# Performance work log

Hardware: AMD Instinct MI355X
Metric: run time of the kernel (lower is better)

## Reference

```python
import jax, jax.numpy as jnp
import numpy as np

B, S, D = 4, 2048, 1024  # batch, seq_len, d_model (h=16 but unused due to source bug)


def setup_inputs() -> dict:
    key = jax.random.key(0)
    ks = jax.random.split(key, 12)
    scale = 1.0 / np.sqrt(D)
    return {
        "q": jax.random.normal(ks[0], (B, S, D), jnp.float32),
        "k": jax.random.normal(ks[1], (B, S, D), jnp.float32),
        "v": jax.random.normal(ks[2], (B, S, D), jnp.float32),
        "mask": jnp.ones((1, 1, S, S), dtype=bool),
        "Wq": jax.random.normal(ks[3], (D, D), jnp.float32) * scale,
        "bq": jnp.zeros((D,), jnp.float32),
        "Wk": jax.random.normal(ks[4], (D, D), jnp.float32) * scale,
        "bk": jnp.zeros((D,), jnp.float32),
        "Wv": jax.random.normal(ks[5], (D, D), jnp.float32) * scale,
        "bv": jnp.zeros((D,), jnp.float32),
        "Wo": jax.random.normal(ks[6], (D, D), jnp.float32) * scale,
        "bo": jnp.zeros((D,), jnp.float32),
    }


def reference(q, k, v, mask, Wq, bq, Wk, bk, Wv, bv, Wo, bo):
    # Faithful to source bugs: head split discarded (attention over full d_model),
    # mask discarded (masked_fill out-of-place), dropout=0 (identity).
    query = q @ Wq + bq  # [B,S,D]
    key = k @ Wk + bk
    value = v @ Wv + bv
    d_k = query.shape[-1]  # = d_model due to the bug
    scores = jnp.einsum('bqd,bkd->bqk', query, key) / jnp.sqrt(jnp.float32(d_k))
    attn = jax.nn.softmax(scores, axis=-1)  # [B,S,S]
    x = jnp.einsum('bqk,bkd->bqd', attn, value)  # [B,S,D]
    # source: x.transpose(1,2).contiguous().view(B,-1,D) -> layout permutation
    b, s, d = x.shape
    x = jnp.swapaxes(x, 1, 2).reshape(b, s, d)
    return x @ Wo + bo
```

## Files before the change

### kernel.cpp

```cpp
#include <hip/hip_runtime.h>
#include <hip/hip_bf16.h>
#include <stdint.h>

typedef __attribute__((ext_vector_type(8))) short short8;
typedef __attribute__((ext_vector_type(4))) float f32x4;
typedef const __attribute__((address_space(1))) uint32_t* gas1_t;
typedef __attribute__((address_space(3))) uint32_t* las3_t;

__device__ __forceinline__ short f2bf(float f) {
  uint32_t u = __builtin_bit_cast(uint32_t, f);
  u += 0x7fffu + ((u >> 16) & 1u);
  return (short)(u >> 16);
}
__device__ __forceinline__ float bf2f(short s) {
  return __builtin_bit_cast(float, ((uint32_t)(uint16_t)s) << 16);
}

__global__ __launch_bounds__(256) void cvt_qkv_k(const float* __restrict__ q,
    const float* __restrict__ k, const float* __restrict__ v,
    short* __restrict__ dst) {
  const long long n = 8388608LL;
  const float* src = (blockIdx.z == 0) ? q : (blockIdx.z == 1) ? k : v;
  long long i = ((long long)blockIdx.x * 256 + threadIdx.x) * 8;
  float4 a = *(const float4*)(src + i);
  float4 b = *(const float4*)(src + i + 4);
  short8 o;
  o[0]=f2bf(a.x); o[1]=f2bf(a.y); o[2]=f2bf(a.z); o[3]=f2bf(a.w);
  o[4]=f2bf(b.x); o[5]=f2bf(b.y); o[6]=f2bf(b.z); o[7]=f2bf(b.w);
  *(short8*)(dst + (long long)blockIdx.z * n + i) = o;
}

__global__ __launch_bounds__(256) void bias_gather_k(const float* b0, const float* b1,
    const float* b2, const float* b3, float* __restrict__ dst) {
  int i = blockIdx.x * 256 + threadIdx.x;
  if (i >= 4096) return;
  int z = i >> 10, j = i & 1023;
  const float* s = (z==0)?b0:(z==1)?b1:(z==2)?b2:b3;
  dst[i] = s[j];
}

__global__ __launch_bounds__(256) void wt_cvt_k(const float* w0, const float* w1,
    const float* w2, const float* w3, short* __restrict__ dst) {
  __shared__ float t[32][33];
  const float* W = (blockIdx.z==0)?w0:(blockIdx.z==1)?w1:(blockIdx.z==2)?w2:w3;
  short* D = dst + (long long)blockIdx.z * 1048576LL;
  int n0 = blockIdx.x * 32, k0 = blockIdx.y * 32;
  int tx = threadIdx.x, ty = threadIdx.y;
  #pragma unroll
  for (int i = 0; i < 4; ++i)
    t[ty + 8*i][tx] = W[(long long)(k0 + ty + 8*i) * 1024 + n0 + tx];
  __syncthreads();
  #pragma unroll
  for (int i = 0; i < 4; ++i)
    D[(long long)(n0 + ty + 8*i) * 1024 + k0 + tx] = f2bf(t[tx][ty + 8*i]);
}

__global__ __launch_bounds__(256) void softmax_bf_k(short* __restrict__ SP) {
  short* sp = SP + (long long)blockIdx.x * 2048;
  const int t = threadIdx.x;
  short8 sv = *(const short8*)(sp + t*8);
  float v[8];
  #pragma unroll
  for (int j = 0; j < 8; ++j) v[j] = bf2f(sv[j]);
  float m = v[0];
  #pragma unroll
  for (int j = 1; j < 8; ++j) m = fmaxf(m, v[j]);
  #pragma unroll
  for (int off = 32; off > 0; off >>= 1) m = fmaxf(m, __shfl_down(m, off, 64));
  __shared__ float rmax[4], rsum[4];
  int wv = t >> 6, ln = t & 63;
  if (ln == 0) rmax[wv] = m;
  __syncthreads();
  m = fmaxf(fmaxf(rmax[0], rmax[1]), fmaxf(rmax[2], rmax[3]));
  float e[8], sum = 0.f;
  #pragma unroll
  for (int j = 0; j < 8; ++j) { e[j] = exp2f((v[j] - m) * 1.44269504f); sum += e[j]; }
  #pragma unroll
  for (int off = 32; off > 0; off >>= 1) sum += __shfl_down(sum, off, 64);
  if (ln == 0) rsum[wv] = sum;
  __syncthreads();
  float inv = 1.0f / (rsum[0] + rsum[1] + rsum[2] + rsum[3]);
  short8 o;
  #pragma unroll
  for (int j = 0; j < 8; ++j) o[j] = f2bf(e[j] * inv);
  *(short8*)(sp + t*8) = o;
}

#define MFMA16(d, a_, b_) d = __builtin_amdgcn_mfma_f32_16x16x32_bf16(a_, b_, d, 0, 0, 0)
#define XCD_DECODE(gxs_, gys_) \
  const int nwg = (int)gridDim.x; \
  const int wg = ((int)blockIdx.x & 7) * (nwg >> 3) + ((int)blockIdx.x >> 3); \
  const int bxi = wg & ((1 << (gxs_)) - 1); \
  const int byi = (wg >> (gxs_)) & ((1 << (gys_)) - 1); \
  const int z = wg >> ((gxs_) + (gys_));

template<int OUT_BF16>
__global__ __launch_bounds__(512, 2) void gemm2_k(const short* __restrict__ A,
    const short* __restrict__ Bt, void* __restrict__ Cv,
    const float* __restrict__ bias,
    int K, int lda, int ldb, int ldc,
    long long sA, long long sB, long long sC, long long sBias,
    float scale, int gxs, int gys)
{
  __shared__ __align__(16) short lds[3][16384];
  XCD_DECODE(gxs, gys);
  A  += (long long)z * sA;
  Bt += (long long)z * sB;
  const int bm = byi * 256;
  const int bn = bxi * 256;
  const int tid  = threadIdx.x;
  const int w    = tid >> 6, lane = tid & 63;
  const int wr   = w >> 2,   wc   = w & 3;
  const int lr   = lane & 15, lk  = lane >> 4;

  const int rsw  = (lk ^ ((lr >> 1) & 3)) * 8;
  const int srow = w * 16 + (lane >> 2);
  const int sg   = ((lane & 3) ^ ((lane >> 3) & 3)) * 8;
  const short* gA[2]; const short* gB[2];
  #pragma unroll
  for (int i = 0; i < 2; ++i) {
    gA[i] = A  + (long long)(bm + i*128 + srow) * lda + sg;
    gB[i] = Bt + (long long)(bn + i*128 + srow) * ldb + sg;
  }

  #define STGA2(buf, i, kt) \
    __builtin_amdgcn_global_load_lds((gas1_t)(gA[i] + (long long)(kt)*32), \
        (las3_t)&lds[buf][(i)*4096 + w*512], 16, 0, 0)
  #define STGB2(buf, i, kt) \
    __builtin_amdgcn_global_load_lds((gas1_t)(gB[i] + (long long)(kt)*32), \
        (las3_t)&lds[buf][8192 + (i)*4096 + w*512], 16, 0, 0)
  #define RDA2(buf, mi) (*(const short8*)&lds[buf][(wr*128 + (mi)*16 + lr)*32 + rsw])
  #define RDB2(buf, ni) (*(const short8*)&lds[buf][8192 + (wc*64 + (ni)*16 + lr)*32 + rsw])

  f32x4 acc[8][4] = {};
  const int nt = K >> 5;

  STGA2(0, 0, 0); STGA2(0, 1, 0); STGB2(0, 0, 0); STGB2(0, 1, 0);
  STGA2(1, 0, 1); STGA2(1, 1, 1); STGB2(1, 0, 1); STGB2(1, 1, 1);
  asm volatile("s_waitcnt vmcnt(4)" ::: "memory");
  __builtin_amdgcn_s_barrier();
  __builtin_amdgcn_sched_barrier(0);

  int b = 0, nb = 2;
  for (int g = 0; g < nt; ++g) {
    short8 aR[8], bR[4];
    #pragma unroll
    for (int mi = 0; mi < 8; ++mi) aR[mi] = RDA2(b, mi);
    #pragma unroll
    for (int ni = 0; ni < 4; ++ni) bR[ni] = RDB2(b, ni);
    if (g + 2 < nt) { STGA2(nb, 0, g+2); STGA2(nb, 1, g+2);
                      STGB2(nb, 0, g+2); STGB2(nb, 1, g+2); }
    #pragma unroll
    for (int mi = 0; mi < 8; ++mi)
      #pragma unroll
      for (int ni = 0; ni < 4; ++ni)
        MFMA16(acc[mi][ni], aR[mi], bR[ni]);
    if (g + 2 < nt)      asm volatile("s_waitcnt vmcnt(4)" ::: "memory");
    else if (g + 1 < nt) asm volatile("s_waitcnt vmcnt(0)" ::: "memory");
    __builtin_amdgcn_s_barrier();
    __builtin_amdgcn_sched_barrier(0);
    b  = (b  == 2) ? 0 : b  + 1;
    nb = (nb == 2) ? 0 : nb + 1;
  }

  const float* bz = bias ? (bias + (long long)z * sBias) : nullptr;
  #pragma unroll
  for (int mi = 0; mi < 8; ++mi) {
    const int row = bm + wr*128 + mi*16 + lk*4;
    #pragma unroll
    for (int ni = 0; ni < 4; ++ni) {
      const int col = bn + wc*64 + ni*16 + lr;
      const float bval = bz ? bz[col] : 0.f;
      #pragma unroll
      for (int r = 0; r < 4; ++r) {
        float val = acc[mi][ni][r] * scale + bval;
        if (OUT_BF16)
          ((short*)Cv)[(long long)z*sC + (long long)(row + r) * ldc + col] = f2bf(val);
        else
          ((float*)Cv)[(long long)z*sC + (long long)(row + r) * ldc + col] = val;
      }
    }
  }
  #undef STGA2
  #undef STGB2
  #undef RDA2
  #undef RDB2
}

template<int OUT_BF16, int BIAS_ROW>
__global__ __launch_bounds__(512, 2) void gemm4_k(const short* __restrict__ A,
    const short* __restrict__ Bt, void* __restrict__ Cv,
    const float* __restrict__ bias,
    int K, int lda, int ldb, int ldc,
    long long sA, long long sB, long long sC, long long sBias,
    float scale, int gxs, int gys)
{
  __shared__ __align__(16) short lds[3][24576];
  XCD_DECODE(gxs, gys);
  A  += (long long)z * sA;
  Bt += (long long)z * sB;
  const int bm = byi * 256;
  const int bn = bxi * 128;
  const int tid  = threadIdx.x;
  const int w    = tid >> 6, lane = tid & 63;
  const int wr   = w >> 1,   wc   = w & 1;
  const int lr   = lane & 15, lk  = lane >> 4;

  const int rsw0 = ((lk    ) ^ (lr & 7)) * 8;
  const int rsw1 = ((lk + 4) ^ (lr & 7)) * 8;
  const int srow = w * 8 + (lane >> 3);
  const int swc  = ((lane & 7) ^ ((lane >> 3) & 7)) * 8;
  const short* gA[4]; const short* gB[2];
  #pragma unroll
  for (int i = 0; i < 4; ++i)
    gA[i] = A + (long long)(bm + i*64 + srow) * lda + swc;
  #pragma unroll
  for (int i = 0; i < 2; ++i)
    gB[i] = Bt + (long long)(bn + i*64 + srow) * ldb + swc;

  #define STGA(buf, i, kt) \
    __builtin_amdgcn_global_load_lds((gas1_t)(gA[i] + (long long)(kt)*64), \
        (las3_t)&lds[buf][(i)*4096 + w*512], 16, 0, 0)
  #define STGB(buf, i, kt) \
    __builtin_amdgcn_global_load_lds((gas1_t)(gB[i] + (long long)(kt)*64), \
        (las3_t)&lds[buf][16384 + (i)*4096 + w*512], 16, 0, 0)
  #define RDA4(buf, mi, ks) (*(const short8*)&lds[buf][(wr*64 + (mi)*16 + lr)*64 + ((ks) ? rsw1 : rsw0)])
  #define RDB4(buf, ni, ks) (*(const short8*)&lds[buf][16384 + (wc*64 + (ni)*16 + lr)*64 + ((ks) ? rsw1 : rsw0)])

  f32x4 acc[4][4] = {};
  const int nt = K >> 6;

  STGA(0, 0, 0); STGA(0, 2, 0); STGB(0, 0, 0);
  STGB(0, 1, 0); STGA(0, 1, 0); STGA(0, 3, 0);
  STGA(1, 0, 1); STGA(1, 2, 1); STGB(1, 0, 1);
  STGB(1, 1, 1); STGA(1, 1, 1); STGA(1, 3, 1);
  asm volatile("s_waitcnt vmcnt(6)" ::: "memory");
  __builtin_amdgcn_s_barrier();
  __builtin_amdgcn_sched_barrier(0);

  int b = 0, nb = 2;
  for (int g = 0; g < nt; ++g) {
    short8 aR[4][2], bR[4][2];
    #pragma unroll
    for (int mi = 0; mi < 4; ++mi) { aR[mi][0] = RDA4(b, mi, 0); aR[mi][1] = RDA4(b, mi, 1); }
    #pragma unroll
    for (int ni = 0; ni < 4; ++ni) { bR[ni][0] = RDB4(b, ni, 0); bR[ni][1] = RDB4(b, ni, 1); }
    if (g + 2 < nt) { STGA(nb, 0, g+2); STGA(nb, 2, g+2); STGB(nb, 0, g+2);
                      STGB(nb, 1, g+2); STGA(nb, 1, g+2); STGA(nb, 3, g+2); }
    #pragma unroll
    for (int mi = 0; mi < 4; ++mi)
      #pragma unroll
      for (int ni = 0; ni < 4; ++ni) {
        MFMA16(acc[mi][ni], aR[mi][0], bR[ni][0]);
        MFMA16(acc[mi][ni], aR[mi][1], bR[ni][1]);
      }
    if (g + 2 < nt)      asm volatile("s_waitcnt vmcnt(6)" ::: "memory");
    else if (g + 1 < nt) asm volatile("s_waitcnt vmcnt(0)" ::: "memory");
    __builtin_amdgcn_s_barrier();
    __builtin_amdgcn_sched_barrier(0);
    b  = (b  == 2) ? 0 : b  + 1;
    nb = (nb == 2) ? 0 : nb + 1;
  }

  const float* bz = bias;
  #pragma unroll
  for (int mi = 0; mi < 4; ++mi) {
    const int row = bm + wr*64 + mi*16 + lk*4;
    #pragma unroll
    for (int ni = 0; ni < 4; ++ni) {
      const int col = bn + wc*64 + ni*16 + lr;
      const float bcol = (bz && !BIAS_ROW) ? bz[(long long)z*sBias + col] : 0.f;
      #pragma unroll
      for (int r = 0; r < 4; ++r) {
        float bval = BIAS_ROW ? bz[row + r] : bcol;
        float val = acc[mi][ni][r] * scale + bval;
        if (OUT_BF16)
          ((short*)Cv)[(long long)z*sC + (long long)(row + r) * ldc + col] = f2bf(val);
        else
          ((float*)Cv)[(long long)z*sC + (long long)(row + r) * ldc + col] = val;
      }
    }
  }
  #undef STGA
  #undef STGB
  #undef RDA4
  #undef RDB4
}

extern "C" void kernel_launch(void* const* d_in, const int* in_sizes, int n_in,
                              void* d_out, int out_size, void* d_ws, size_t ws_size,
                              hipStream_t stream) {
  const float* q  = (const float*)d_in[0];
  const float* k  = (const float*)d_in[1];
  const float* v  = (const float*)d_in[2];
  const float* Wq = (const float*)d_in[4];
  const float* bq = (const float*)d_in[5];
  const float* Wk = (const float*)d_in[6];
  const float* bk = (const float*)d_in[7];
  const float* Wv = (const float*)d_in[8];
  const float* bv = (const float*)d_in[9];
  const float* Wo = (const float*)d_in[10];
  const float* bo = (const float*)d_in[11];

  char* w = (char*)d_ws;
  short* Wt     = (short*)(w);
  float* biasb  = (float*)(w + 8388608);
  short* QKV    = (short*)(w + 8404992);
  short* qkvbf  = (short*)(w + 58736640);
  short* P      = (short*)(w + 58736640);
  short* Vt     = (short*)(w + 109068288);
  short* xt     = (short*)(w + 125845504);

  short* Qp = QKV;
  short* Kp = QKV + 8388608LL;
  short* vbf = qkvbf + 16777216LL;

  cvt_qkv_k<<<dim3(4096,1,3), 256, 0, stream>>>(q, k, v, qkvbf);
  bias_gather_k<<<dim3(16), 256, 0, stream>>>(bq, bk, bv, bo, biasb);
  wt_cvt_k<<<dim3(32,32,4), dim3(32,8), 0, stream>>>(Wq, Wk, Wv, Wo, Wt);

  gemm2_k<1><<<256, 512, 0, stream>>>(qkvbf, Wt, QKV, biasb,
      1024, 1024, 1024, 1024, 8388608LL, 1048576LL, 8388608LL, 1024LL, 1.0f, 2, 5);

  gemm4_k<1,1><<<256, 512, 0, stream>>>(Wt + 2097152LL, vbf, Vt, biasb + 2048,
      1024, 1024, 1024, 8192, 0LL, 0LL, 0LL, 0LL, 1.0f, 6, 2);

  gemm2_k<1><<<256, 512, 0, stream>>>(Qp, Kp, P, nullptr,
      1024, 1024, 1024, 2048, 2097152LL, 2097152LL, 4194304LL, 0LL, 0.03125f, 3, 3);

  softmax_bf_k<<<dim3(8192), 256, 0, stream>>>(P);

  gemm4_k<1,0><<<256, 512, 0, stream>>>(Vt, P, xt, nullptr,
      2048, 8192, 2048, 2048, 2048LL, 4194304LL, 2097152LL, 0LL, 1.0f, 4, 2);

  gemm4_k<0,0><<<256, 512, 0, stream>>>(xt, Wt + 3145728LL, (float*)d_out,
      biasb + 3072, 1024, 1024, 1024, 1024, 2097152LL, 0LL, 2097152LL, 0LL, 1.0f, 3, 3);
}
```

Measured before the change: 207.9 us.

## Fuse fp32-to-bf16 input conversion into QKV projection GEMM loads

Removes the separate cvt_qkv_k pass over q, k and v. New GEMM variants load the fp32 activations straight into LDS and convert them to bf16 in registers before the MFMA. This avoids writing and re-reading about 50 MB of bf16 intermediates. In exchange each GEMM moves twice the bytes per A/B tile through LDS and does conversion work in the inner loop, which may cost occupancy or MFMA throughput.

```diff
diff --git a/kernel.cpp b/kernel.cpp
--- a/kernel.cpp
+++ b/kernel.cpp
@@ -15,19 +15,11 @@
 __device__ __forceinline__ float bf2f(short s) {
   return __builtin_bit_cast(float, ((uint32_t)(uint16_t)s) << 16);
 }
-
-__global__ __launch_bounds__(256) void cvt_qkv_k(const float* __restrict__ q,
-    const float* __restrict__ k, const float* __restrict__ v,
-    short* __restrict__ dst) {
-  const long long n = 8388608LL;
-  const float* src = (blockIdx.z == 0) ? q : (blockIdx.z == 1) ? k : v;
-  long long i = ((long long)blockIdx.x * 256 + threadIdx.x) * 8;
-  float4 a = *(const float4*)(src + i);
-  float4 b = *(const float4*)(src + i + 4);
-  short8 o;
-  o[0]=f2bf(a.x); o[1]=f2bf(a.y); o[2]=f2bf(a.z); o[3]=f2bf(a.w);
-  o[4]=f2bf(b.x); o[5]=f2bf(b.y); o[6]=f2bf(b.z); o[7]=f2bf(b.w);
-  *(short8*)(dst + (long long)blockIdx.z * n + i) = o;
+__device__ __forceinline__ short8 cvt8(float4 a, float4 b) {
+  short8 s;
+  s[0]=f2bf(a.x); s[1]=f2bf(a.y); s[2]=f2bf(a.z); s[3]=f2bf(a.w);
+  s[4]=f2bf(b.x); s[5]=f2bf(b.y); s[6]=f2bf(b.z); s[7]=f2bf(b.w);
+  return s;
 }
 
 __global__ __launch_bounds__(256) void bias_gather_k(const float* b0, const float* b1,
@@ -187,6 +179,179 @@
   #undef RDB2
 }
 
+__global__ __launch_bounds__(512, 2) void gemm2f_k(
+    const float* __restrict__ A0p, const float* __restrict__ A1p,
+    const short* __restrict__ Bt, short* __restrict__ C,
+    const float* __restrict__ bias,
+    int K, int lda, int ldb, int ldc,
+    long long sB, long long sC, long long sBias,
+    float scale, int gxs, int gys)
+{
+  __shared__ __align__(16) short lds[3][24576];
+  XCD_DECODE(gxs, gys);
+  const float* Af = z ? A1p : A0p;
+  const int bm = byi * 256;
+  const int bn = bxi * 256;
+  const int tid  = threadIdx.x;
+  const int w    = tid >> 6, lane = tid & 63;
+  const int wr   = w >> 2,   wc   = w & 3;
+  const int lr   = lane & 15, lk  = lane >> 4;
+
+  const int sarow = w * 8 + (lane >> 3);
+  const int sag   = ((lane & 7) ^ ((lane >> 3) & 7)) * 4;
+  const int sbrow = w * 16 + (lane >> 2);
+  const int sbg   = ((lane & 3) ^ ((lane >> 3) & 3)) * 8;
+  const int rswb  = (lk ^ ((lr >> 1) & 3)) * 8;
+  const float* gAf[4]; const short* gB[2];
+  #pragma unroll
+  for (int i = 0; i < 4; ++i)
+    gAf[i] = Af + (long long)(bm + i*64 + sarow) * lda + sag;
+  #pragma unroll
+  for (int i = 0; i < 2; ++i)
+    gB[i] = Bt + (long long)z * sB + (long long)(bn + i*128 + sbrow) * ldb + sbg;
+
+  #define STGAF(buf, i, kt) \
+    __builtin_amdgcn_global_load_lds((gas1_t)(gAf[i] + (long long)(kt)*32), \
+        (las3_t)&lds[buf][(i)*4096 + w*512], 16, 0, 0)
+  #define STGBF(buf, i, kt) \
+    __builtin_amdgcn_global_load_lds((gas1_t)(gB[i] + (long long)(kt)*32), \
+        (las3_t)&lds[buf][16384 + (i)*4096 + w*512], 16, 0, 0)
+  #define RDAF(buf, mi, j) (*(const float4*)&lds[buf][(wr*128 + (mi)*16 + lr)*64 + ((2*lk + (j)) ^ (lr & 7))*8])
+  #define RDBF(buf, ni) (*(const short8*)&lds[buf][16384 + (wc*64 + (ni)*16 + lr)*32 + rswb])
+
+  f32x4 acc[8][4] = {};
+  const int nt = K >> 5;
+
+  STGAF(0,0,0); STGAF(0,1,0); STGAF(0,2,0); STGAF(0,3,0); STGBF(0,0,0); STGBF(0,1,0);
+  STGAF(1,0,1); STGAF(1,1,1); STGAF(1,2,1); STGAF(1,3,1); STGBF(1,0,1); STGBF(1,1,1);
+  asm volatile("s_waitcnt vmcnt(6)" ::: "memory");
+  __builtin_amdgcn_s_barrier();
+  __builtin_amdgcn_sched_barrier(0);
+
+  int b = 0, nb = 2;
+  for (int g = 0; g < nt; ++g) {
+    short8 aR[8], bR[4];
+    #pragma unroll
+    for (int mi = 0; mi < 8; ++mi) aR[mi] = cvt8(RDAF(b, mi, 0), RDAF(b, mi, 1));
+    #pragma unroll
+    for (int ni = 0; ni < 4; ++ni) bR[ni] = RDBF(b, ni);
+    if (g + 2 < nt) { STGAF(nb,0,g+2); STGAF(nb,1,g+2); STGAF(nb,2,g+2);
+                      STGAF(nb,3,g+2); STGBF(nb,0,g+2); STGBF(nb,1,g+2); }
+    #pragma unroll
+    for (int mi = 0; mi < 8; ++mi)
+      #pragma unroll
+      for (int ni = 0; ni < 4; ++ni)
+        MFMA16(acc[mi][ni], aR[mi], bR[ni]);
+    if (g + 2 < nt)      asm volatile("s_waitcnt vmcnt(6)" ::: "memory");
+    else if (g + 1 < nt) asm volatile("s_waitcnt vmcnt(0)" ::: "memory");
+    __builtin_amdgcn_s_barrier();
+    __builtin_amdgcn_sched_barrier(0);
+    b  = (b  == 2) ? 0 : b  + 1;
+    nb = (nb == 2) ? 0 : nb + 1;
+  }
+
+  const float* bz = bias + (long long)z * sBias;
+  #pragma unroll
+  for (int mi = 0; mi < 8; ++mi) {
+    const int row = bm + wr*128 + mi*16 + lk*4;
+    #pragma unroll
+    for (int ni = 0; ni < 4; ++ni) {
+      const int col = bn + wc*64 + ni*16 + lr;
+      const float bval = bz[col];
+      #pragma unroll
+      for (int r = 0; r < 4; ++r)
+        C[(long long)z*sC + (long long)(row + r) * ldc + col] = f2bf(acc[mi][ni][r] * scale + bval);
+    }
+  }
+  #undef STGAF
+  #undef STGBF
+  #undef RDAF
+  #undef RDBF
+}
+
+__global__ __launch_bounds__(512, 2) void gemm4f_k(
+    const short* __restrict__ A, const float* __restrict__ Btf,
+    short* __restrict__ C, const float* __restrict__ bias,
+    int K, int lda, int ldb, int ldc, float scale, int gxs, int gys)
+{
+  __shared__ __align__(16) short lds[3][16384];
+  XCD_DECODE(gxs, gys);
+  (void)z;
+  const int bm = byi * 256;
+  const int bn = bxi * 128;
+  const int tid  = threadIdx.x;
+  const int w    = tid >> 6, lane = tid & 63;
+  const int wr   = w >> 1,   wc   = w & 1;
+  const int lr   = lane & 15, lk  = lane >> 4;
+
+  const int sarow = w * 16 + (lane >> 2);
+  const int sag   = ((lane & 3) ^ ((lane >> 3) & 3)) * 8;
+  const int rswa  = (lk ^ ((lr >> 1) & 3)) * 8;
+  const int sbrow = w * 8 + (lane >> 3);
+  const int sbg   = ((lane & 7) ^ ((lane >> 3) & 7)) * 4;
+  const short* gA[2]; const float* gBf[2];
+  #pragma unroll
+  for (int i = 0; i < 2; ++i) {
+    gA[i]  = A   + (long long)(bm + i*128 + sarow) * lda + sag;
+    gBf[i] = Btf + (long long)(bn + i*64  + sbrow) * ldb + sbg;
+  }
+
+  #define STGA4(buf, i, kt) \
+    __builtin_amdgcn_global_load_lds((gas1_t)(gA[i] + (long long)(kt)*32), \
+        (las3_t)&lds[buf][(i)*4096 + w*512], 16, 0, 0)
+  #define STGB4(buf, i, kt) \
+    __builtin_amdgcn_global_load_lds((gas1_t)(gBf[i] + (long long)(kt)*32), \
+        (las3_t)&lds[buf][8192 + (i)*4096 + w*512], 16, 0, 0)
+  #define RDA4F(buf, mi) (*(const short8*)&lds[buf][(wr*64 + (mi)*16 + lr)*32 + rswa])
+  #define RDB4F(buf, ni, j) (*(const float4*)&lds[buf][8192 + (wc*64 + (ni)*16 + lr)*64 + ((2*lk + (j)) ^ (lr & 7))*8])
+
+  f32x4 acc[4][4] = {};
+  const int nt = K >> 5;
+
+  STGA4(0,0,0); STGA4(0,1,0); STGB4(0,0,0); STGB4(0,1,0);
+  STGA4(1,0,1); STGA4(1,1,1); STGB4(1,0,1); STGB4(1,1,1);
+  asm volatile("s_waitcnt vmcnt(4)" ::: "memory");
+  __builtin_amdgcn_s_barrier();
+  __builtin_amdgcn_sched_barrier(0);
+
+  int b = 0, nb = 2;
+  for (int g = 0; g < nt; ++g) {
+    short8 aR[4], bR[4];
+    #pragma unroll
+    for (int mi = 0; mi < 4; ++mi) aR[mi] = RDA4F(b, mi);
+    #pragma unroll
+    for (int ni = 0; ni < 4; ++ni) bR[ni] = cvt8(RDB4F(b, ni, 0), RDB4F(b, ni, 1));
+    if (g + 2 < nt) { STGA4(nb,0,g+2); STGA4(nb,1,g+2); STGB4(nb,0,g+2); STGB4(nb,1,g+2); }
+    #pragma unroll
+    for (int mi = 0; mi < 4; ++mi)
+      #pragma unroll
+      for (int ni = 0; ni < 4; ++ni)
+        MFMA16(acc[mi][ni], aR[mi], bR[ni]);
+    if (g + 2 < nt)      asm volatile("s_waitcnt vmcnt(4)" ::: "memory");
+    else if (g + 1 < nt) asm volatile("s_waitcnt vmcnt(0)" ::: "memory");
+    __builtin_amdgcn_s_barrier();
+    __builtin_amdgcn_sched_barrier(0);
+    b  = (b  == 2) ? 0 : b  + 1;
+    nb = (nb == 2) ? 0 : nb + 1;
+  }
+
+  #pragma unroll
+  for (int mi = 0; mi < 4; ++mi) {
+    const int row = bm + wr*64 + mi*16 + lk*4;
+    #pragma unroll
+    for (int ni = 0; ni < 4; ++ni) {
+      const int col = bn + wc*64 + ni*16 + lr;
+      #pragma unroll
+      for (int r = 0; r < 4; ++r)
+        C[(long long)(row + r) * ldc + col] = f2bf(acc[mi][ni][r] * scale + bias[row + r]);
+    }
+  }
+  #undef STGA4
+  #undef STGB4
+  #undef RDA4F
+  #undef RDB4F
+}
+
 template<int OUT_BF16, int BIAS_ROW>
 __global__ __launch_bounds__(512, 2) void gemm4_k(const short* __restrict__ A,
     const short* __restrict__ Bt, void* __restrict__ Cv,
@@ -306,24 +471,21 @@
   short* Wt     = (short*)(w);
   float* biasb  = (float*)(w + 8388608);
   short* QKV    = (short*)(w + 8404992);
-  short* qkvbf  = (short*)(w + 58736640);
   short* P      = (short*)(w + 58736640);
   short* Vt     = (short*)(w + 109068288);
   short* xt     = (short*)(w + 125845504);
 
   short* Qp = QKV;
   short* Kp = QKV + 8388608LL;
-  short* vbf = qkvbf + 16777216LL;
-
-  cvt_qkv_k<<<dim3(4096,1,3), 256, 0, stream>>>(q, k, v, qkvbf);
+
   bias_gather_k<<<dim3(16), 256, 0, stream>>>(bq, bk, bv, bo, biasb);
   wt_cvt_k<<<dim3(32,32,4), dim3(32,8), 0, stream>>>(Wq, Wk, Wv, Wo, Wt);
 
-  gemm2_k<1><<<256, 512, 0, stream>>>(qkvbf, Wt, QKV, biasb,
-      1024, 1024, 1024, 1024, 8388608LL, 1048576LL, 8388608LL, 1024LL, 1.0f, 2, 5);
-
-  gemm4_k<1,1><<<256, 512, 0, stream>>>(Wt + 2097152LL, vbf, Vt, biasb + 2048,
-      1024, 1024, 1024, 8192, 0LL, 0LL, 0LL, 0LL, 1.0f, 6, 2);
+  gemm2f_k<<<256, 512, 0, stream>>>(q, k, Wt, QKV, biasb,
+      1024, 1024, 1024, 1024, 1048576LL, 8388608LL, 1024LL, 1.0f, 2, 5);
+
+  gemm4f_k<<<256, 512, 0, stream>>>(Wt + 2097152LL, v, Vt, biasb + 2048,
+      1024, 1024, 1024, 8192, 1.0f, 6, 2);
 
   gemm2_k<1><<<256, 512, 0, stream>>>(Qp, Kp, P, nullptr,
       1024, 1024, 1024, 2048, 2097152LL, 2097152LL, 4194304LL, 0LL, 0.03125f, 3, 3);
```

Measured after the change: 218.9 us. +5.3%, slower.

## Rework gemm4 main loop to K=32 tiles with 4-stage ring and register double-buffering

Applied to the files above, without the earlier changes.

Replaces the 256x128 GEMM's 3-buffer K=64 LDS pipeline with a 4-buffer ring of K=32 tiles, a new XOR swizzle, and even/odd register double-buffering. The LDS reads for the next tile are issued before the MFMAs of the current one, so read latency overlaps with math. LDS use drops from 144KB to 96KB per block. The cost is twice as many barriers per unit of K, and the smaller per-iteration global loads may expose more load latency.

```diff
diff --git a/kernel.cpp b/kernel.cpp
--- a/kernel.cpp
+++ b/kernel.cpp
@@ -188,14 +188,14 @@
 }
 
 template<int OUT_BF16, int BIAS_ROW>
-__global__ __launch_bounds__(512, 2) void gemm4_k(const short* __restrict__ A,
+__global__ __launch_bounds__(512, 2) void gemm4r_k(const short* __restrict__ A,
     const short* __restrict__ Bt, void* __restrict__ Cv,
     const float* __restrict__ bias,
     int K, int lda, int ldb, int ldc,
     long long sA, long long sB, long long sC, long long sBias,
     float scale, int gxs, int gys)
 {
-  __shared__ __align__(16) short lds[3][24576];
+  __shared__ __align__(16) short lds[4][12288];
   XCD_DECODE(gxs, gys);
   A  += (long long)z * sA;
   Bt += (long long)z * sB;
@@ -206,60 +206,72 @@
   const int wr   = w >> 1,   wc   = w & 1;
   const int lr   = lane & 15, lk  = lane >> 4;
 
-  const int rsw0 = ((lk    ) ^ (lr & 7)) * 8;
-  const int rsw1 = ((lk + 4) ^ (lr & 7)) * 8;
-  const int srow = w * 8 + (lane >> 3);
-  const int swc  = ((lane & 7) ^ ((lane >> 3) & 7)) * 8;
-  const short* gA[4]; const short* gB[2];
-  #pragma unroll
-  for (int i = 0; i < 4; ++i)
-    gA[i] = A + (long long)(bm + i*64 + srow) * lda + swc;
-  #pragma unroll
-  for (int i = 0; i < 2; ++i)
-    gB[i] = Bt + (long long)(bn + i*64 + srow) * ldb + swc;
-
-  #define STGA(buf, i, kt) \
-    __builtin_amdgcn_global_load_lds((gas1_t)(gA[i] + (long long)(kt)*64), \
-        (las3_t)&lds[buf][(i)*4096 + w*512], 16, 0, 0)
-  #define STGB(buf, i, kt) \
-    __builtin_amdgcn_global_load_lds((gas1_t)(gB[i] + (long long)(kt)*64), \
-        (las3_t)&lds[buf][16384 + (i)*4096 + w*512], 16, 0, 0)
-  #define RDA4(buf, mi, ks) (*(const short8*)&lds[buf][(wr*64 + (mi)*16 + lr)*64 + ((ks) ? rsw1 : rsw0)])
-  #define RDB4(buf, ni, ks) (*(const short8*)&lds[buf][16384 + (wc*64 + (ni)*16 + lr)*64 + ((ks) ? rsw1 : rsw0)])
+  const int rsw  = (lk ^ ((lr >> 1) & 3)) * 8;
+  const int srow = w * 16 + (lane >> 2);
+  const int sg   = ((lane & 3) ^ ((lane >> 3) & 3)) * 8;
+  const short* gA[2]; const short* gB;
+  #pragma unroll
+  for (int h = 0; h < 2; ++h)
+    gA[h] = A + (long long)(bm + h*128 + srow) * lda + sg;
+  gB = Bt + (long long)(bn + srow) * ldb + sg;
+
+  #define STGAr(buf, h, kt) \
+    __builtin_amdgcn_global_load_lds((gas1_t)(gA[h] + (long long)(kt)*32), \
+        (las3_t)&lds[buf][(h)*4096 + w*512], 16, 0, 0)
+  #define STGBr(buf, kt) \
+    __builtin_amdgcn_global_load_lds((gas1_t)(gB + (long long)(kt)*32), \
+        (las3_t)&lds[buf][8192 + w*512], 16, 0, 0)
+  #define RDAr(buf, mi) (*(const short8*)&lds[buf][(wr*64 + (mi)*16 + lr)*32 + rsw])
+  #define RDBr(buf, ni) (*(const short8*)&lds[buf][8192 + (wc*64 + (ni)*16 + lr)*32 + rsw])
 
   f32x4 acc[4][4] = {};
-  const int nt = K >> 6;
-
-  STGA(0, 0, 0); STGA(0, 2, 0); STGB(0, 0, 0);
-  STGB(0, 1, 0); STGA(0, 1, 0); STGA(0, 3, 0);
-  STGA(1, 0, 1); STGA(1, 2, 1); STGB(1, 0, 1);
-  STGB(1, 1, 1); STGA(1, 1, 1); STGA(1, 3, 1);
-  asm volatile("s_waitcnt vmcnt(6)" ::: "memory");
+  const int nt = K >> 5;
+
+  STGAr(0, 0, 0); STGAr(0, 1, 0); STGBr(0, 0);
+  STGAr(1, 0, 1); STGAr(1, 1, 1); STGBr(1, 1);
+  asm volatile("s_waitcnt vmcnt(3)" ::: "memory");
   __builtin_amdgcn_s_barrier();
   __builtin_amdgcn_sched_barrier(0);
 
-  int b = 0, nb = 2;
-  for (int g = 0; g < nt; ++g) {
-    short8 aR[4][2], bR[4][2];
-    #pragma unroll
-    for (int mi = 0; mi < 4; ++mi) { aR[mi][0] = RDA4(b, mi, 0); aR[mi][1] = RDA4(b, mi, 1); }
-    #pragma unroll
-    for (int ni = 0; ni < 4; ++ni) { bR[ni][0] = RDB4(b, ni, 0); bR[ni][1] = RDB4(b, ni, 1); }
-    if (g + 2 < nt) { STGA(nb, 0, g+2); STGA(nb, 2, g+2); STGB(nb, 0, g+2);
-                      STGB(nb, 1, g+2); STGA(nb, 1, g+2); STGA(nb, 3, g+2); }
-    #pragma unroll
-    for (int mi = 0; mi < 4; ++mi)
-      #pragma unroll
-      for (int ni = 0; ni < 4; ++ni) {
-        MFMA16(acc[mi][ni], aR[mi][0], bR[ni][0]);
-        MFMA16(acc[mi][ni], aR[mi][1], bR[ni][1]);
+  short8 aE[4], bE[4], aO[4], bO[4];
+  #pragma unroll
+  for (int i = 0; i < 4; ++i) { aE[i] = RDAr(0, i); bE[i] = RDBr(0, i); }
+
+  for (int g = 0; g < nt; g += 2) {
+    {
+      const int bs = (g + 2) & 3;
+      if (g + 2 < nt) { STGAr(bs, 0, g+2); STGAr(bs, 1, g+2); STGBr(bs, g+2); }
+      if (g + 2 < nt)      asm volatile("s_waitcnt vmcnt(3)" ::: "memory");
+      else                 asm volatile("s_waitcnt vmcnt(0)" ::: "memory");
+      __builtin_amdgcn_s_barrier();
+      __builtin_amdgcn_sched_barrier(0);
+      const int br = (g + 1) & 3;
+      #pragma unroll
+      for (int i = 0; i < 4; ++i) { aO[i] = RDAr(br, i); bO[i] = RDBr(br, i); }
+      #pragma unroll
+      for (int mi = 0; mi < 4; ++mi)
+        #pragma unroll
+        for (int ni = 0; ni < 4; ++ni)
+          MFMA16(acc[mi][ni], aE[mi], bE[ni]);
+    }
+    {
+      const int bs = (g + 3) & 3;
+      if (g + 3 < nt) { STGAr(bs, 0, g+3); STGAr(bs, 1, g+3); STGBr(bs, g+3); }
+      if (g + 3 < nt)      asm volatile("s_waitcnt vmcnt(3)" ::: "memory");
+      else if (g + 2 < nt) asm volatile("s_waitcnt vmcnt(0)" ::: "memory");
+      __builtin_amdgcn_s_barrier();
+      __builtin_amdgcn_sched_barrier(0);
+      if (g + 2 < nt) {
+        const int br = (g + 2) & 3;
+        #pragma unroll
+        for (int i = 0; i < 4; ++i) { aE[i] = RDAr(br, i); bE[i] = RDBr(br, i); }
       }
-    if (g + 2 < nt)      asm volatile("s_waitcnt vmcnt(6)" ::: "memory");
-    else if (g + 1 < nt) asm volatile("s_waitcnt vmcnt(0)" ::: "memory");
-    __builtin_amdgcn_s_barrier();
-    __builtin_amdgcn_sched_barrier(0);
-    b  = (b  == 2) ? 0 : b  + 1;
-    nb = (nb == 2) ? 0 : nb + 1;
+      #pragma unroll
+      for (int mi = 0; mi < 4; ++mi)
+        #pragma unroll
+        for (int ni = 0; ni < 4; ++ni)
+          MFMA16(acc[mi][ni], aO[mi], bO[ni]);
+    }
   }
 
   const float* bz = bias;
@@ -281,10 +293,10 @@
       }
     }
   }
-  #undef STGA
-  #undef STGB
-  #undef RDA4
-  #undef RDB4
+  #undef STGAr
+  #undef STGBr
+  #undef RDAr
+  #undef RDBr
 }
 
 extern "C" void kernel_launch(void* const* d_in, const int* in_sizes, int n_in,
@@ -322,7 +334,7 @@
   gemm2_k<1><<<256, 512, 0, stream>>>(qkvbf, Wt, QKV, biasb,
       1024, 1024, 1024, 1024, 8388608LL, 1048576LL, 8388608LL, 1024LL, 1.0f, 2, 5);
 
-  gemm4_k<1,1><<<256, 512, 0, stream>>>(Wt + 2097152LL, vbf, Vt, biasb + 2048,
+  gemm4r_k<1,1><<<256, 512, 0, stream>>>(Wt + 2097152LL, vbf, Vt, biasb + 2048,
       1024, 1024, 1024, 8192, 0LL, 0LL, 0LL, 0LL, 1.0f, 6, 2);
 
   gemm2_k<1><<<256, 512, 0, stream>>>(Qp, Kp, P, nullptr,
@@ -330,9 +342,9 @@
 
   softmax_bf_k<<<dim3(8192), 256, 0, stream>>>(P);
 
-  gemm4_k<1,0><<<256, 512, 0, stream>>>(Vt, P, xt, nullptr,
+  gemm4r_k<1,0><<<256, 512, 0, stream>>>(Vt, P, xt, nullptr,
       2048, 8192, 2048, 2048, 2048LL, 4194304LL, 2097152LL, 0LL, 1.0f, 4, 2);
 
-  gemm4_k<0,0><<<256, 512, 0, stream>>>(xt, Wt + 3145728LL, (float*)d_out,
+  gemm4r_k<0,0><<<256, 512, 0, stream>>>(xt, Wt + 3145728LL, (float*)d_out,
       biasb + 3072, 1024, 1024, 1024, 1024, 2097152LL, 0LL, 2097152LL, 0LL, 1.0f, 3, 3);
 }
```

Measured after the change: 214.9 us. 3.4% more time.
